# Optimization experiments

Measured on AMD Instinct MI355X. Metric: run time of the kernel, lower is better.

The kernel has to match this reference:

```python
import jax, jax.numpy as jnp
import numpy as np

B, T, D_IN, D_OUT, H = 2, 2048, 1024, 1024, 16
HD = D_OUT // H


def setup_inputs() -> dict:
    key = jax.random.key(0)
    ks = jax.random.split(key, 6)
    s_in = 1.0 / np.sqrt(D_IN)
    s_out = 1.0 / np.sqrt(D_OUT)
    return {
        "x": jax.random.normal(ks[0], (B, T, D_IN), dtype=jnp.float32),
        # torch nn.Linear stores weight as (out_features, in_features)
        "Wq": jax.random.uniform(ks[1], (D_OUT, D_IN), jnp.float32, -s_in, s_in),
        "Wk": jax.random.uniform(ks[2], (D_OUT, D_IN), jnp.float32, -s_in, s_in),
        "Wv": jax.random.uniform(ks[3], (D_OUT, D_IN), jnp.float32, -s_in, s_in),
        "Wo": jax.random.uniform(ks[4], (D_OUT, D_OUT), jnp.float32, -s_out, s_out),
        "bo": jax.random.uniform(ks[5], (D_OUT,), jnp.float32, -s_out, s_out),
    }


def reference(x, Wq, Wk, Wv, Wo, bo):
    b, t, _ = x.shape
    q = jnp.einsum("btd,ed->bte", x, Wq).reshape(b, t, H, HD).transpose(0, 2, 1, 3)
    k = jnp.einsum("btd,ed->bte", x, Wk).reshape(b, t, H, HD).transpose(0, 2, 1, 3)
    v = jnp.einsum("btd,ed->bte", x, Wv).reshape(b, t, H, HD).transpose(0, 2, 1, 3)
    # [b, h, q, k] materialized scores, masked then scaled (as in source)
    scores = jnp.einsum("bhqd,bhkd->bhqk", q, k)
    causal = jnp.triu(jnp.ones((t, t), dtype=bool), k=1)
    scores = jnp.where(causal, -jnp.inf, scores)
    attn = jax.nn.softmax(scores / jnp.sqrt(jnp.float32(HD)), axis=-1)
    ctx = jnp.einsum("bhqk,bhkd->bhqd", attn, v)
    # NOTE: the source does .view(b, t, d_out) WITHOUT transposing (b,h,t,hd)
    # back to (b,t,h,hd). We replicate that reshape faithfully.
    ctx = ctx.reshape(b, t, D_OUT)
    return jnp.einsum("btd,ed->bte", ctx, Wo) + bo
```

## Files before the change

kernel.cpp:

```cpp
#include <hip/hip_runtime.h>
#include <math.h>

#define BB 2
#define TT 2048
#define DD 1024
#define NH 16
#define HDD 64

typedef __attribute__((ext_vector_type(8))) short v8s;
typedef __attribute__((ext_vector_type(4))) short v4s;
typedef __attribute__((ext_vector_type(4))) float f32x4;

__device__ __forceinline__ unsigned short f2bf(float f) {
    union { float f; unsigned int u; } c; c.f = f;
    unsigned int r = c.u + 0x7FFF + ((c.u >> 16) & 1);
    return (unsigned short)(r >> 16);
}

__device__ __forceinline__ v4s pack_bf16x4(float a, float b, float c, float d) {
#if __has_builtin(__builtin_amdgcn_cvt_pk_bf16_f32)
    auto lo = __builtin_amdgcn_cvt_pk_bf16_f32(a, b);
    auto hi = __builtin_amdgcn_cvt_pk_bf16_f32(c, d);
    union { v4s v; struct { decltype(lo) l; decltype(hi) h; } p; } u;
    u.p.l = lo; u.p.h = hi;
    return u.v;
#else
    v4s r;
    r[0] = (short)f2bf(a); r[1] = (short)f2bf(b);
    r[2] = (short)f2bf(c); r[3] = (short)f2bf(d);
    return r;
#endif
}

__device__ __forceinline__ float fexp2(float x) {
#if __has_builtin(__builtin_amdgcn_exp2f)
    return __builtin_amdgcn_exp2f(x);
#else
    float r; asm("v_exp_f32 %0, %1" : "=v"(r) : "v"(x)); return r;
#endif
}

__device__ __forceinline__ void gload_lds16(const void* g, void* l) {
    __builtin_amdgcn_global_load_lds(
        (const __attribute__((address_space(1))) void*)g,
        (__attribute__((address_space(3))) void*)l, 16, 0, 0);
}

__device__ __forceinline__ f32x4 mfma16x16x16bf16(v4s a, v4s b, f32x4 c) {
#if __has_builtin(__builtin_amdgcn_mfma_f32_16x16x16bf16_1k)
    return __builtin_amdgcn_mfma_f32_16x16x16bf16_1k(a, b, c, 0, 0, 0);
#else
    f32x4 d;
    asm("v_mfma_f32_16x16x16_bf16 %0, %1, %2, %0"
        : "=v"(d) : "v"(a), "v"(b), "0"(c));
    return d;
#endif
}

__global__ __launch_bounds__(256) void cast5_kernel(
    const float* __restrict__ x, const float* __restrict__ wq,
    const float* __restrict__ wk, const float* __restrict__ wv,
    const float* __restrict__ wo,
    unsigned short* __restrict__ xo, unsigned short* __restrict__ wqo,
    unsigned short* __restrict__ wko, unsigned short* __restrict__ wvo,
    unsigned short* __restrict__ woo)
{
    const int tid = blockIdx.x * 256 + threadIdx.x;
    if (blockIdx.y == 0) {
        const int n4 = BB * TT * DD / 4;
#pragma unroll
        for (int p = 0; p < 4; ++p) {
            const int i = tid + (p << 18);
            if (i < n4) {
                float4 v = ((const float4*)x)[i];
                ushort4 o;
                o.x = f2bf(v.x); o.y = f2bf(v.y); o.z = f2bf(v.z); o.w = f2bf(v.w);
                ((ushort4*)xo)[i] = o;
            }
        }
    } else {
        const float* s; unsigned short* d;
        switch (blockIdx.y) {
            case 1: s = wq; d = wqo; break;
            case 2: s = wk; d = wko; break;
            case 3: s = wv; d = wvo; break;
            default: s = wo; d = woo; break;
        }
        float4 v = ((const float4*)s)[tid];
        ushort4 o;
        o.x = f2bf(v.x); o.y = f2bf(v.y); o.z = f2bf(v.z); o.w = f2bf(v.w);
        ((ushort4*)d)[tid] = o;
    }
}

__global__ __launch_bounds__(256, 3) void qkv_mfma(
    const unsigned short* __restrict__ x,
    const unsigned short* __restrict__ wq, const unsigned short* __restrict__ wk,
    const unsigned short* __restrict__ wv,
    unsigned short* __restrict__ qo, unsigned short* __restrict__ ko,
    unsigned short* __restrict__ vo)
{
    __shared__ unsigned short SMEM[24576];

    const int tid = threadIdx.x;
    const int lane = tid & 63;
    const int wid = tid >> 6;
    const int l15 = lane & 15, quad = lane >> 4;
    const int l7 = l15 & 7;

    const int m0 = blockIdx.x << 7;
    const int ny = blockIdx.y;
    const int which = ny >> 4;
    const int n0 = (ny & 15) << 6;
    const unsigned short* W = (which == 0) ? wq : (which == 1) ? wk : wv;

    const int wm = (wid >> 1) << 6;
    const int wn = (wid & 1) << 5;

    char* const smem = (char*)SMEM;

#define QKV_STAGE(k0, buf)                                                     \
    do {                                                                       \
        _Pragma("unroll") for (int p = 0; p < 4; ++p) {                        \
            const int f = (tid << 4) + (p << 12);                              \
            const int r = f >> 7;                                              \
            const int gc = ((((f >> 4) & 7) ^ (r & 7)) << 3);                  \
            gload_lds16(&x[(size_t)(m0 + r) * DD + (k0) + gc],                 \
                        smem + (buf) * 16384 + f);                             \
        }                                                                      \
        _Pragma("unroll") for (int p = 0; p < 2; ++p) {                        \
            const int f = (tid << 4) + (p << 12);                              \
            const int r = f >> 7;                                              \
            const int gc = ((((f >> 4) & 7) ^ (r & 7)) << 3);                  \
            gload_lds16(&W[(size_t)(n0 + r) * DD + (k0) + gc],                 \
                        smem + 32768 + (buf) * 8192 + f);                      \
        }                                                                      \
    } while (0)

    f32x4 acc[4][2] = {};

    QKV_STAGE(0, 0);
    __syncthreads();

    int cur = 0;
    for (int k0 = 0; k0 < DD; k0 += 64) {
        if (k0 + 64 < DD) QKV_STAGE(k0 + 64, cur ^ 1);

        const char* Ab = smem + cur * 16384;
        const char* Bb = smem + 32768 + cur * 8192;
#pragma unroll
        for (int h = 0; h < 2; ++h) {
            const int rc = (((h << 2) + quad) ^ l7) << 4;
            v8s af[4], bf[2];
#pragma unroll
            for (int i = 0; i < 4; ++i)
                af[i] = *(const v8s*)(Ab + (wm + (i << 4) + l15) * 128 + rc);
#pragma unroll
            for (int j = 0; j < 2; ++j)
                bf[j] = *(const v8s*)(Bb + (wn + (j << 4) + l15) * 128 + rc);
#pragma unroll
            for (int i = 0; i < 4; ++i)
#pragma unroll
                for (int j = 0; j < 2; ++j)
                    acc[i][j] = __builtin_amdgcn_mfma_f32_16x16x32_bf16(
                        af[i], bf[j], acc[i][j], 0, 0, 0);
        }

        __syncthreads();
        cur ^= 1;
    }
#undef QKV_STAGE

    if (which == 2) {
#pragma unroll
        for (int i = 0; i < 4; ++i)
#pragma unroll
            for (int j = 0; j < 2; ++j) {
                const int n = n0 + wn + (j << 4) + l15;
                const int h = n >> 6, hd = n & 63;
                const int mb = m0 + wm + (i << 4) + (quad << 2);
                const int b = mb >> 11, t = mb & 2047;
                ushort4 pk;
                pk.x = f2bf(acc[i][j][0]); pk.y = f2bf(acc[i][j][1]);
                pk.z = f2bf(acc[i][j][2]); pk.w = f2bf(acc[i][j][3]);
                *(ushort4*)&vo[((((size_t)(b * NH + h) << 6) + hd) << 11) + t] = pk;
            }
    } else {
        unsigned short* outp = (which == 0) ? qo : ko;
        const float sc = (which == 1) ? 0.18033688011112042f : 1.0f;
#pragma unroll
        for (int p = 0; p < 2; ++p) {
            __syncthreads();
            if ((wid >> 1) == p) {
#pragma unroll
                for (int i = 0; i < 4; ++i)
#pragma unroll
                    for (int j = 0; j < 2; ++j)
#pragma unroll
                        for (int r = 0; r < 4; ++r) {
                            const int row = (i << 4) + (quad << 2) + r;
                            SMEM[row * 72 + wn + (j << 4) + l15] = f2bf(acc[i][j][r] * sc);
                        }
            }
            __syncthreads();
            const int rr = tid >> 2;
            const int cg = (tid & 3) << 4;
            const int m = m0 + (p << 6) + rr;
            const int b = m >> 11, t = m & 2047;
#pragma unroll
            for (int k2 = 0; k2 < 2; ++k2) {
                const int col = cg + (k2 << 3);
                const int n = n0 + col;
                const int h = n >> 6, hd = n & 63;
                const uint4 val = *(const uint4*)&SMEM[rr * 72 + col];
                *(uint4*)&outp[(((size_t)(b * NH + h) * TT + t) << 6) + hd] = val;
            }
        }
    }
}

__global__ __launch_bounds__(256) void attn_mfma(
    const unsigned short* __restrict__ q, const unsigned short* __restrict__ k,
    const unsigned short* __restrict__ vt, unsigned short* __restrict__ ctx)
{
    __shared__ unsigned short Qs[64][64];
    __shared__ unsigned short Ks[2][64][64];
    __shared__ unsigned short Vts[2][64][64];

    const int tid = threadIdx.x;
    const int lane = tid & 63;
    const int wid = tid >> 6;
    const int l15 = lane & 15, quad = lane >> 4;
    const int r7 = (l15 & 7) << 3;

    const int bh = blockIdx.x;
    const int qt = 31 - (int)blockIdx.y;
    const int q0 = qt << 6;
    const int qrow = q0 + (wid << 4) + l15;

    const unsigned short* qb = q + (size_t)bh * TT * HDD;
    const unsigned short* kb = k + (size_t)bh * TT * HDD;
    const unsigned short* vb = vt + (size_t)bh * HDD * TT;
    unsigned short* cb = ctx + (size_t)bh * TT * HDD;

    const int cr = tid >> 3;
    const int cc = (tid & 7) << 3;
    const int cs = cc ^ ((cr & 7) << 3);

#pragma unroll
    for (int u = 0; u < 2; ++u) {
        const int r = cr + (u << 5);
        *(uint4*)&Qs[r][cs] = *(const uint4*)&qb[(size_t)(q0 + r) * HDD + cc];
    }
    {
        uint4 k0r = *(const uint4*)&kb[(size_t)cr * HDD + cc];
        uint4 k1r = *(const uint4*)&kb[(size_t)(cr + 32) * HDD + cc];
        uint4 v0r = *(const uint4*)&vb[((size_t)cr << 11) + cc];
        uint4 v1r = *(const uint4*)&vb[((size_t)(cr + 32) << 11) + cc];
        *(uint4*)&Ks[0][cr][cs] = k0r;
        *(uint4*)&Ks[0][cr + 32][cs] = k1r;
        *(uint4*)&Vts[0][cr][cs] = v0r;
        *(uint4*)&Vts[0][cr + 32][cs] = v1r;
    }
    __syncthreads();

    v8s qf[2];
#pragma unroll
    for (int c = 0; c < 2; ++c)
        qf[c] = *(const v8s*)&Qs[(wid << 4) + l15]
                               [(((c << 5) + (quad << 3)) ^ r7)];

    float m_i = -INFINITY, l_i = 0.f;
    f32x4 o[4] = {};

    for (int jt = 0; jt <= qt; ++jt) {
        const int cur = jt & 1;

        uint4 k0r, k1r, v0r, v1r;
        const bool pre = (jt < qt);
        if (pre) {
            const int kn = (jt + 1) << 6;
            k0r = *(const uint4*)&kb[(size_t)(kn + cr) * HDD + cc];
            k1r = *(const uint4*)&kb[(size_t)(kn + cr + 32) * HDD + cc];
            v0r = *(const uint4*)&vb[((size_t)cr << 11) + kn + cc];
            v1r = *(const uint4*)&vb[((size_t)(cr + 32) << 11) + kn + cc];
        }

        const int k0 = jt << 6;

        f32x4 s[4] = {};
        const int kc0 = (quad << 3) ^ r7;
#pragma unroll
        for (int m = 0; m < 4; ++m) {
            const v8s kf0 = *(const v8s*)&Ks[cur][(m << 4) + l15][kc0];
            const v8s kf1 = *(const v8s*)&Ks[cur][(m << 4) + l15][kc0 ^ 32];
            s[m] = __builtin_amdgcn_mfma_f32_16x16x32_bf16(kf0, qf[0], s[m], 0, 0, 0);
            s[m] = __builtin_amdgcn_mfma_f32_16x16x32_bf16(kf1, qf[1], s[m], 0, 0, 0);
        }

        if (jt == qt) {
#pragma unroll
            for (int m = 0; m < 4; ++m) {
                const int kc = k0 + (m << 4) + (quad << 2);
#pragma unroll
                for (int r = 0; r < 4; ++r)
                    if (kc + r > qrow) s[m][r] = -INFINITY;
            }
        }

        float mx = fmaxf(fmaxf(s[0][0], s[0][1]), fmaxf(s[0][2], s[0][3]));
        mx = fmaxf(mx, fmaxf(fmaxf(s[1][0], s[1][1]), fmaxf(s[1][2], s[1][3])));
        mx = fmaxf(mx, fmaxf(fmaxf(s[2][0], s[2][1]), fmaxf(s[2][2], s[2][3])));
        mx = fmaxf(mx, fmaxf(fmaxf(s[3][0], s[3][1]), fmaxf(s[3][2], s[3][3])));
        mx = fmaxf(mx, __shfl_xor(mx, 16));
        mx = fmaxf(mx, __shfl_xor(mx, 32));
        const float m_new = fmaxf(m_i, mx);
        const float alpha = fexp2(m_i - m_new);
        m_i = m_new;

        float sum = 0.f;
        v4s pf[4];
#pragma unroll
        for (int m = 0; m < 4; ++m) {
            const float p0 = fexp2(s[m][0] - m_new);
            const float p1 = fexp2(s[m][1] - m_new);
            const float p2 = fexp2(s[m][2] - m_new);
            const float p3 = fexp2(s[m][3] - m_new);
            sum += (p0 + p1) + (p2 + p3);
            pf[m] = pack_bf16x4(p0, p1, p2, p3);
        }
        sum += __shfl_xor(sum, 16);
        sum += __shfl_xor(sum, 32);
        l_i = l_i * alpha + sum;

#pragma unroll
        for (int m = 0; m < 4; ++m)
#pragma unroll
            for (int r = 0; r < 4; ++r)
                o[m][r] *= alpha;

#pragma unroll
        for (int m = 0; m < 4; ++m)
#pragma unroll
            for (int c = 0; c < 4; ++c) {
                const v4s vf = *(const v4s*)&Vts[cur][(m << 4) + l15]
                                                    [(((c << 4) + (quad << 2)) ^ r7)];
                o[m] = mfma16x16x16bf16(vf, pf[c], o[m]);
            }

        if (pre) {
            const int nxt = cur ^ 1;
            *(uint4*)&Ks[nxt][cr][cs] = k0r;
            *(uint4*)&Ks[nxt][cr + 32][cs] = k1r;
            *(uint4*)&Vts[nxt][cr][cs] = v0r;
            *(uint4*)&Vts[nxt][cr + 32][cs] = v1r;
        }
        __syncthreads();
    }

    const float linv = 1.f / l_i;
#pragma unroll
    for (int m = 0; m < 4; ++m) {
        ushort4 st;
        st.x = f2bf(o[m][0] * linv); st.y = f2bf(o[m][1] * linv);
        st.z = f2bf(o[m][2] * linv); st.w = f2bf(o[m][3] * linv);
        *(ushort4*)&cb[((size_t)qrow << 6) + (m << 4) + (quad << 2)] = st;
    }
}

__global__ __launch_bounds__(256, 3) void oproj_mfma(
    const unsigned short* __restrict__ c, const unsigned short* __restrict__ wo,
    const float* __restrict__ bo, float* __restrict__ out)
{
    __shared__ unsigned short SMEM[24576];

    const int tid = threadIdx.x;
    const int lane = tid & 63;
    const int wid = tid >> 6;
    const int l15 = lane & 15, quad = lane >> 4;
    const int l7 = l15 & 7;

    const int m0 = blockIdx.x << 7;
    const int n0 = blockIdx.y << 6;
    const int wm = (wid >> 1) << 6;
    const int wn = (wid & 1) << 5;

    char* const smem = (char*)SMEM;

#define OP_STAGE(k0, buf)                                                      \
    do {                                                                       \
        _Pragma("unroll") for (int p = 0; p < 4; ++p) {                        \
            const int f = (tid << 4) + (p << 12);                              \
            const int r = f >> 7;                                              \
            const int gc = ((((f >> 4) & 7) ^ (r & 7)) << 3);                  \
            gload_lds16(&c[(size_t)(m0 + r) * DD + (k0) + gc],                 \
                        smem + (buf) * 16384 + f);                             \
        }                                                                      \
        _Pragma("unroll") for (int p = 0; p < 2; ++p) {                        \
            const int f = (tid << 4) + (p << 12);                              \
            const int r = f >> 7;                                              \
            const int gc = ((((f >> 4) & 7) ^ (r & 7)) << 3);                  \
            gload_lds16(&wo[(size_t)(n0 + r) * DD + (k0) + gc],                \
                        smem + 32768 + (buf) * 8192 + f);                      \
        }                                                                      \
    } while (0)

    f32x4 acc[4][2] = {};

    OP_STAGE(0, 0);
    __syncthreads();

    int cur = 0;
    for (int k0 = 0; k0 < DD; k0 += 64) {
        if (k0 + 64 < DD) OP_STAGE(k0 + 64, cur ^ 1);

        const char* Ab = smem + cur * 16384;
        const char* Bb = smem + 32768 + cur * 8192;
#pragma unroll
        for (int h = 0; h < 2; ++h) {
            const int rc = (((h << 2) + quad) ^ l7) << 4;
            v8s af[4], bf[2];
#pragma unroll
            for (int i = 0; i < 4; ++i)
                af[i] = *(const v8s*)(Ab + (wm + (i << 4) + l15) * 128 + rc);
#pragma unroll
            for (int j = 0; j < 2; ++j)
                bf[j] = *(const v8s*)(Bb + (wn + (j << 4) + l15) * 128 + rc);
#pragma unroll
            for (int i = 0; i < 4; ++i)
#pragma unroll
                for (int j = 0; j < 2; ++j)
                    acc[i][j] = __builtin_amdgcn_mfma_f32_16x16x32_bf16(
                        af[i], bf[j], acc[i][j], 0, 0, 0);
        }

        __syncthreads();
        cur ^= 1;
    }
#undef OP_STAGE

#pragma unroll
    for (int j = 0; j < 2; ++j) {
        const int n = n0 + wn + (j << 4) + l15;
        const float bias = bo[n];
#pragma unroll
        for (int i = 0; i < 4; ++i) {
            const int mb = m0 + wm + (i << 4) + (quad << 2);
#pragma unroll
            for (int r = 0; r < 4; ++r)
                out[(size_t)(mb + r) * DD + n] = acc[i][j][r] + bias;
        }
    }
}

extern "C" void kernel_launch(void* const* d_in, const int* in_sizes, int n_in,
                              void* d_out, int out_size, void* d_ws, size_t ws_size,
                              hipStream_t stream) {
    const float* x  = (const float*)d_in[0];
    const float* Wq = (const float*)d_in[1];
    const float* Wk = (const float*)d_in[2];
    const float* Wv = (const float*)d_in[3];
    const float* Wo = (const float*)d_in[4];
    const float* bo = (const float*)d_in[5];
    float* out = (float*)d_out;

    const size_t NX = (size_t)BB * TT * DD;
    const size_t NW = (size_t)DD * DD;

    unsigned short* xb  = (unsigned short*)d_ws;
    unsigned short* wqb = xb + NX;
    unsigned short* wkb = wqb + NW;
    unsigned short* wvb = wkb + NW;
    unsigned short* wob = wvb + NW;
    unsigned short* qb  = wob + NW;
    unsigned short* kb  = qb + NX;
    unsigned short* vtb = kb + NX;
    unsigned short* cbuf = vtb + NX;

    cast5_kernel<<<dim3(1024, 5), 256, 0, stream>>>(x, Wq, Wk, Wv, Wo,
                                                    xb, wqb, wkb, wvb, wob);
    qkv_mfma<<<dim3(32, 48), 256, 0, stream>>>(xb, wqb, wkb, wvb, qb, kb, vtb);
    attn_mfma<<<dim3(32, 32), 256, 0, stream>>>(qb, kb, vtb, cbuf);
    oproj_mfma<<<dim3(32, 16), 256, 0, stream>>>(cbuf, wob, bo, out);
}
```

Before: 169.3 us.

## Widen attention key/value tile to 128 and load Q fragments from global

The attention kernel now processes 128 keys per iteration instead of 64. This halves the number of loop iterations, barriers and online-softmax rescale steps per query tile. The K/V shared buffers double in size and get new XOR swizzles, and the staging loads move into macros. Q fragments are read straight from global memory into registers rather than through a shared-memory tile. In exchange, LDS per block grows to 64KB and register pressure rises, which can lower occupancy, and the last block wastes work on fully masked keys when the query tile index is even.

Result: slower. 217.1 us (+28.3%).

```diff
diff --git a/kernel.cpp b/kernel.cpp
--- a/kernel.cpp
+++ b/kernel.cpp
@@ -223,19 +223,20 @@
     const unsigned short* __restrict__ q, const unsigned short* __restrict__ k,
     const unsigned short* __restrict__ vt, unsigned short* __restrict__ ctx)
 {
-    __shared__ unsigned short Qs[64][64];
-    __shared__ unsigned short Ks[2][64][64];
-    __shared__ unsigned short Vts[2][64][64];
+    __shared__ unsigned short Ks[2][128][64];
+    __shared__ unsigned short Vts[2][64][128];
 
     const int tid = threadIdx.x;
     const int lane = tid & 63;
     const int wid = tid >> 6;
     const int l15 = lane & 15, quad = lane >> 4;
     const int r7 = (l15 & 7) << 3;
+    const int rv = l15 << 3;
 
     const int bh = blockIdx.x;
     const int qt = 31 - (int)blockIdx.y;
     const int q0 = qt << 6;
+    const int nkb = (qt >> 1) + 1;
     const int qrow = q0 + (wid << 4) + l15;
 
     const unsigned short* qb = q + (size_t)bh * TT * HDD;
@@ -243,75 +244,76 @@
     const unsigned short* vb = vt + (size_t)bh * HDD * TT;
     unsigned short* cb = ctx + (size_t)bh * TT * HDD;
 
-    const int cr = tid >> 3;
-    const int cc = (tid & 7) << 3;
-    const int cs = cc ^ ((cr & 7) << 3);
-
-#pragma unroll
-    for (int u = 0; u < 2; ++u) {
-        const int r = cr + (u << 5);
-        *(uint4*)&Qs[r][cs] = *(const uint4*)&qb[(size_t)(q0 + r) * HDD + cc];
-    }
-    {
-        uint4 k0r = *(const uint4*)&kb[(size_t)cr * HDD + cc];
-        uint4 k1r = *(const uint4*)&kb[(size_t)(cr + 32) * HDD + cc];
-        uint4 v0r = *(const uint4*)&vb[((size_t)cr << 11) + cc];
-        uint4 v1r = *(const uint4*)&vb[((size_t)(cr + 32) << 11) + cc];
-        *(uint4*)&Ks[0][cr][cs] = k0r;
-        *(uint4*)&Ks[0][cr + 32][cs] = k1r;
-        *(uint4*)&Vts[0][cr][cs] = v0r;
-        *(uint4*)&Vts[0][cr + 32][cs] = v1r;
-    }
+    uint4 kr[4], vr[4];
+
+#define ATT_LOAD(kn)                                                           \
+    do {                                                                       \
+        _Pragma("unroll") for (int p = 0; p < 4; ++p) {                        \
+            const int f = (tid << 4) + (p << 12);                              \
+            const int krow = f >> 7, kch = (f >> 4) & 7;                       \
+            const int vrow = f >> 8, vch = (f >> 4) & 15;                      \
+            kr[p] = *(const uint4*)&kb[(size_t)((kn) + krow) * HDD + (kch << 3)]; \
+            vr[p] = *(const uint4*)&vb[((size_t)vrow << 11) + (kn) + (vch << 3)]; \
+        }                                                                      \
+    } while (0)
+
+#define ATT_PUBLISH(buf)                                                       \
+    do {                                                                       \
+        _Pragma("unroll") for (int p = 0; p < 4; ++p) {                        \
+            const int f = (tid << 4) + (p << 12);                              \
+            const int krow = f >> 7, kch = (f >> 4) & 7;                       \
+            const int vrow = f >> 8, vch = (f >> 4) & 15;                      \
+            *(uint4*)&Ks[buf][krow][(kch ^ (krow & 7)) << 3] = kr[p];          \
+            *(uint4*)&Vts[buf][vrow][(vch ^ (vrow & 15)) << 3] = vr[p];        \
+        }                                                                      \
+    } while (0)
+
+    ATT_LOAD(0);
+    ATT_PUBLISH(0);
+
+    v8s qf[2];
+#pragma unroll
+    for (int c = 0; c < 2; ++c)
+        qf[c] = *(const v8s*)&qb[(size_t)(q0 + (wid << 4) + l15) * HDD
+                                 + (c << 5) + (quad << 3)];
+
     __syncthreads();
-
-    v8s qf[2];
-#pragma unroll
-    for (int c = 0; c < 2; ++c)
-        qf[c] = *(const v8s*)&Qs[(wid << 4) + l15]
-                               [(((c << 5) + (quad << 3)) ^ r7)];
 
     float m_i = -INFINITY, l_i = 0.f;
     f32x4 o[4] = {};
 
-    for (int jt = 0; jt <= qt; ++jt) {
-        const int cur = jt & 1;
-
-        uint4 k0r, k1r, v0r, v1r;
-        const bool pre = (jt < qt);
-        if (pre) {
-            const int kn = (jt + 1) << 6;
-            k0r = *(const uint4*)&kb[(size_t)(kn + cr) * HDD + cc];
-            k1r = *(const uint4*)&kb[(size_t)(kn + cr + 32) * HDD + cc];
-            v0r = *(const uint4*)&vb[((size_t)cr << 11) + kn + cc];
-            v1r = *(const uint4*)&vb[((size_t)(cr + 32) << 11) + kn + cc];
-        }
-
-        const int k0 = jt << 6;
-
-        f32x4 s[4] = {};
+    for (int jb = 0; jb < nkb; ++jb) {
+        const int cur = jb & 1;
+        const bool pre = (jb + 1 < nkb);
+        if (pre) ATT_LOAD((jb + 1) << 7);
+
+        f32x4 s[8];
         const int kc0 = (quad << 3) ^ r7;
 #pragma unroll
-        for (int m = 0; m < 4; ++m) {
-            const v8s kf0 = *(const v8s*)&Ks[cur][(m << 4) + l15][kc0];
-            const v8s kf1 = *(const v8s*)&Ks[cur][(m << 4) + l15][kc0 ^ 32];
-            s[m] = __builtin_amdgcn_mfma_f32_16x16x32_bf16(kf0, qf[0], s[m], 0, 0, 0);
-            s[m] = __builtin_amdgcn_mfma_f32_16x16x32_bf16(kf1, qf[1], s[m], 0, 0, 0);
-        }
-
-        if (jt == qt) {
-#pragma unroll
-            for (int m = 0; m < 4; ++m) {
-                const int kc = k0 + (m << 4) + (quad << 2);
+        for (int mk = 0; mk < 8; ++mk) {
+            const v8s kf0 = *(const v8s*)&Ks[cur][(mk << 4) + l15][kc0];
+            const v8s kf1 = *(const v8s*)&Ks[cur][(mk << 4) + l15][kc0 ^ 32];
+            f32x4 t = {};
+            t = __builtin_amdgcn_mfma_f32_16x16x32_bf16(kf0, qf[0], t, 0, 0, 0);
+            t = __builtin_amdgcn_mfma_f32_16x16x32_bf16(kf1, qf[1], t, 0, 0, 0);
+            s[mk] = t;
+        }
+
+        if (jb == nkb - 1) {
+#pragma unroll
+            for (int mk = 0; mk < 8; ++mk) {
+                const int kc = (jb << 7) + (mk << 4) + (quad << 2);
 #pragma unroll
                 for (int r = 0; r < 4; ++r)
-                    if (kc + r > qrow) s[m][r] = -INFINITY;
-            }
-        }
-
-        float mx = fmaxf(fmaxf(s[0][0], s[0][1]), fmaxf(s[0][2], s[0][3]));
-        mx = fmaxf(mx, fmaxf(fmaxf(s[1][0], s[1][1]), fmaxf(s[1][2], s[1][3])));
-        mx = fmaxf(mx, fmaxf(fmaxf(s[2][0], s[2][1]), fmaxf(s[2][2], s[2][3])));
-        mx = fmaxf(mx, fmaxf(fmaxf(s[3][0], s[3][1]), fmaxf(s[3][2], s[3][3])));
+                    if (kc + r > qrow) s[mk][r] = -INFINITY;
+            }
+        }
+
+        float mx = -INFINITY;
+#pragma unroll
+        for (int mk = 0; mk < 8; ++mk)
+            mx = fmaxf(mx, fmaxf(fmaxf(s[mk][0], s[mk][1]),
+                                 fmaxf(s[mk][2], s[mk][3])));
         mx = fmaxf(mx, __shfl_xor(mx, 16));
         mx = fmaxf(mx, __shfl_xor(mx, 32));
         const float m_new = fmaxf(m_i, mx);
@@ -319,15 +321,15 @@
         m_i = m_new;
 
         float sum = 0.f;
-        v4s pf[4];
-#pragma unroll
-        for (int m = 0; m < 4; ++m) {
-            const float p0 = fexp2(s[m][0] - m_new);
-            const float p1 = fexp2(s[m][1] - m_new);
-            const float p2 = fexp2(s[m][2] - m_new);
-            const float p3 = fexp2(s[m][3] - m_new);
+        v4s pf[8];
+#pragma unroll
+        for (int mk = 0; mk < 8; ++mk) {
+            const float p0 = fexp2(s[mk][0] - m_new);
+            const float p1 = fexp2(s[mk][1] - m_new);
+            const float p2 = fexp2(s[mk][2] - m_new);
+            const float p3 = fexp2(s[mk][3] - m_new);
             sum += (p0 + p1) + (p2 + p3);
-            pf[m] = pack_bf16x4(p0, p1, p2, p3);
+            pf[mk] = pack_bf16x4(p0, p1, p2, p3);
         }
         sum += __shfl_xor(sum, 16);
         sum += __shfl_xor(sum, 32);
@@ -342,21 +344,17 @@
 #pragma unroll
         for (int m = 0; m < 4; ++m)
 #pragma unroll
-            for (int c = 0; c < 4; ++c) {
+            for (int c = 0; c < 8; ++c) {
                 const v4s vf = *(const v4s*)&Vts[cur][(m << 4) + l15]
-                                                    [(((c << 4) + (quad << 2)) ^ r7)];
+                                                    [(((c << 4) + (quad << 2)) ^ rv)];
                 o[m] = mfma16x16x16bf16(vf, pf[c], o[m]);
             }
 
-        if (pre) {
-            const int nxt = cur ^ 1;
-            *(uint4*)&Ks[nxt][cr][cs] = k0r;
-            *(uint4*)&Ks[nxt][cr + 32][cs] = k1r;
-            *(uint4*)&Vts[nxt][cr][cs] = v0r;
-            *(uint4*)&Vts[nxt][cr + 32][cs] = v1r;
-        }
+        if (pre) ATT_PUBLISH(cur ^ 1);
         __syncthreads();
     }
+#undef ATT_LOAD
+#undef ATT_PUBLISH
 
     const float linv = 1.f / l_i;
 #pragma unroll
```

## Unroll attention loop by two, use max3, MFMA row sums and setprio

Applied to the files above, without the earlier changes.

Unrolls the attention key-tile loop by two so the double-buffer index becomes a compile-time constant. It replaces the fmaxf reduction tree with v_max3_f32 inline asm and computes the softmax row sum with MFMAs against a ones vector instead of VALU adds plus shuffles. It also raises wave priority around the MFMA blocks with s_setprio. These moves shift work from VALU to the matrix unit and help interleave waves, at the cost of more code size and register pressure.

Result: no change. 171.3 us (+1.2%).

```diff
diff --git a/kernel.cpp b/kernel.cpp
--- a/kernel.cpp
+++ b/kernel.cpp
@@ -40,6 +40,12 @@
 #endif
 }
 
+__device__ __forceinline__ float fmax3(float a, float b, float c) {
+    float d;
+    asm("v_max3_f32 %0, %1, %2, %3" : "=v"(d) : "v"(a), "v"(b), "v"(c));
+    return d;
+}
+
 __device__ __forceinline__ void gload_lds16(const void* g, void* l) {
     __builtin_amdgcn_global_load_lds(
         (const __attribute__((address_space(1))) void*)g,
@@ -270,93 +276,94 @@
         qf[c] = *(const v8s*)&Qs[(wid << 4) + l15]
                                [(((c << 5) + (quad << 3)) ^ r7)];
 
+    const v4s vones = {0x3F80, 0x3F80, 0x3F80, 0x3F80};
     float m_i = -INFINITY, l_i = 0.f;
     f32x4 o[4] = {};
-
-    for (int jt = 0; jt <= qt; ++jt) {
-        const int cur = jt & 1;
-
-        uint4 k0r, k1r, v0r, v1r;
-        const bool pre = (jt < qt);
-        if (pre) {
-            const int kn = (jt + 1) << 6;
-            k0r = *(const uint4*)&kb[(size_t)(kn + cr) * HDD + cc];
-            k1r = *(const uint4*)&kb[(size_t)(kn + cr + 32) * HDD + cc];
-            v0r = *(const uint4*)&vb[((size_t)cr << 11) + kn + cc];
-            v1r = *(const uint4*)&vb[((size_t)(cr + 32) << 11) + kn + cc];
-        }
-
-        const int k0 = jt << 6;
-
-        f32x4 s[4] = {};
-        const int kc0 = (quad << 3) ^ r7;
-#pragma unroll
-        for (int m = 0; m < 4; ++m) {
-            const v8s kf0 = *(const v8s*)&Ks[cur][(m << 4) + l15][kc0];
-            const v8s kf1 = *(const v8s*)&Ks[cur][(m << 4) + l15][kc0 ^ 32];
-            s[m] = __builtin_amdgcn_mfma_f32_16x16x32_bf16(kf0, qf[0], s[m], 0, 0, 0);
-            s[m] = __builtin_amdgcn_mfma_f32_16x16x32_bf16(kf1, qf[1], s[m], 0, 0, 0);
-        }
-
-        if (jt == qt) {
-#pragma unroll
-            for (int m = 0; m < 4; ++m) {
-                const int kc = k0 + (m << 4) + (quad << 2);
-#pragma unroll
-                for (int r = 0; r < 4; ++r)
-                    if (kc + r > qrow) s[m][r] = -INFINITY;
-            }
-        }
-
-        float mx = fmaxf(fmaxf(s[0][0], s[0][1]), fmaxf(s[0][2], s[0][3]));
-        mx = fmaxf(mx, fmaxf(fmaxf(s[1][0], s[1][1]), fmaxf(s[1][2], s[1][3])));
-        mx = fmaxf(mx, fmaxf(fmaxf(s[2][0], s[2][1]), fmaxf(s[2][2], s[2][3])));
-        mx = fmaxf(mx, fmaxf(fmaxf(s[3][0], s[3][1]), fmaxf(s[3][2], s[3][3])));
-        mx = fmaxf(mx, __shfl_xor(mx, 16));
-        mx = fmaxf(mx, __shfl_xor(mx, 32));
-        const float m_new = fmaxf(m_i, mx);
-        const float alpha = fexp2(m_i - m_new);
-        m_i = m_new;
-
-        float sum = 0.f;
-        v4s pf[4];
-#pragma unroll
-        for (int m = 0; m < 4; ++m) {
-            const float p0 = fexp2(s[m][0] - m_new);
-            const float p1 = fexp2(s[m][1] - m_new);
-            const float p2 = fexp2(s[m][2] - m_new);
-            const float p3 = fexp2(s[m][3] - m_new);
-            sum += (p0 + p1) + (p2 + p3);
-            pf[m] = pack_bf16x4(p0, p1, p2, p3);
-        }
-        sum += __shfl_xor(sum, 16);
-        sum += __shfl_xor(sum, 32);
-        l_i = l_i * alpha + sum;
-
-#pragma unroll
-        for (int m = 0; m < 4; ++m)
-#pragma unroll
-            for (int r = 0; r < 4; ++r)
-                o[m][r] *= alpha;
-
-#pragma unroll
-        for (int m = 0; m < 4; ++m)
-#pragma unroll
-            for (int c = 0; c < 4; ++c) {
-                const v4s vf = *(const v4s*)&Vts[cur][(m << 4) + l15]
-                                                    [(((c << 4) + (quad << 2)) ^ r7)];
-                o[m] = mfma16x16x16bf16(vf, pf[c], o[m]);
-            }
-
-        if (pre) {
-            const int nxt = cur ^ 1;
-            *(uint4*)&Ks[nxt][cr][cs] = k0r;
-            *(uint4*)&Ks[nxt][cr + 32][cs] = k1r;
-            *(uint4*)&Vts[nxt][cr][cs] = v0r;
-            *(uint4*)&Vts[nxt][cr + 32][cs] = v1r;
-        }
-        __syncthreads();
-    }
+    const int kc0 = (quad << 3) ^ r7;
+
+#define ATT_BODY(JT, CUR)                                                      \
+    {                                                                          \
+        uint4 k0r, k1r, v0r, v1r;                                              \
+        const bool pre = ((JT) < qt);                                          \
+        if (pre) {                                                             \
+            const int kn = ((JT) + 1) << 6;                                    \
+            k0r = *(const uint4*)&kb[(size_t)(kn + cr) * HDD + cc];            \
+            k1r = *(const uint4*)&kb[(size_t)(kn + cr + 32) * HDD + cc];       \
+            v0r = *(const uint4*)&vb[((size_t)cr << 11) + kn + cc];            \
+            v1r = *(const uint4*)&vb[((size_t)(cr + 32) << 11) + kn + cc];     \
+        }                                                                      \
+        f32x4 s[4] = {};                                                       \
+        __builtin_amdgcn_s_setprio(1);                                         \
+        _Pragma("unroll") for (int m = 0; m < 4; ++m) {                        \
+            const v8s kf0 = *(const v8s*)&Ks[CUR][(m << 4) + l15][kc0];        \
+            const v8s kf1 = *(const v8s*)&Ks[CUR][(m << 4) + l15][kc0 ^ 32];   \
+            s[m] = __builtin_amdgcn_mfma_f32_16x16x32_bf16(kf0, qf[0], s[m], 0, 0, 0); \
+            s[m] = __builtin_amdgcn_mfma_f32_16x16x32_bf16(kf1, qf[1], s[m], 0, 0, 0); \
+        }                                                                      \
+        __builtin_amdgcn_s_setprio(0);                                         \
+        if ((JT) == qt) {                                                      \
+            _Pragma("unroll") for (int m = 0; m < 4; ++m) {                    \
+                const int kc = ((JT) << 6) + (m << 4) + (quad << 2);           \
+                _Pragma("unroll") for (int r = 0; r < 4; ++r)                  \
+                    if (kc + r > qrow) s[m][r] = -INFINITY;                    \
+            }                                                                  \
+        }                                                                      \
+        float mx = fmax3(s[0][0], s[0][1], s[0][2]);                           \
+        float mb2 = fmax3(s[0][3], s[1][0], s[1][1]);                          \
+        float mb3 = fmax3(s[1][2], s[1][3], s[2][0]);                          \
+        float mb4 = fmax3(s[2][1], s[2][2], s[2][3]);                          \
+        float mb5 = fmax3(s[3][0], s[3][1], s[3][2]);                          \
+        mx = fmax3(mx, mb2, mb3);                                              \
+        mb4 = fmax3(mb4, mb5, s[3][3]);                                        \
+        mx = fmaxf(mx, mb4);                                                   \
+        mx = fmaxf(mx, __shfl_xor(mx, 16));                                    \
+        mx = fmaxf(mx, __shfl_xor(mx, 32));                                    \
+        const float m_new = fmaxf(m_i, mx);                                    \
+        const float alpha = fexp2(m_i - m_new);                                \
+        m_i = m_new;                                                           \
+        v4s pf[4];                                                             \
+        _Pragma("unroll") for (int m = 0; m < 4; ++m) {                        \
+            const float p0 = fexp2(s[m][0] - m_new);                           \
+            const float p1 = fexp2(s[m][1] - m_new);                           \
+            const float p2 = fexp2(s[m][2] - m_new);                           \
+            const float p3 = fexp2(s[m][3] - m_new);                           \
+            pf[m] = pack_bf16x4(p0, p1, p2, p3);                               \
+        }                                                                      \
+        f32x4 ls = {};                                                         \
+        ls = mfma16x16x16bf16(vones, pf[0], ls);                               \
+        ls = mfma16x16x16bf16(vones, pf[1], ls);                               \
+        ls = mfma16x16x16bf16(vones, pf[2], ls);                               \
+        ls = mfma16x16x16bf16(vones, pf[3], ls);                               \
+        l_i = l_i * alpha + ls[0];                                             \
+        _Pragma("unroll") for (int m = 0; m < 4; ++m)                          \
+            _Pragma("unroll") for (int r = 0; r < 4; ++r)                      \
+                o[m][r] *= alpha;                                              \
+        __builtin_amdgcn_s_setprio(1);                                         \
+        _Pragma("unroll") for (int m = 0; m < 4; ++m)                          \
+            _Pragma("unroll") for (int c = 0; c < 4; ++c) {                    \
+                const v4s vf = *(const v4s*)&Vts[CUR][(m << 4) + l15]          \
+                                   [(((c << 4) + (quad << 2)) ^ r7)];          \
+                o[m] = mfma16x16x16bf16(vf, pf[c], o[m]);                      \
+            }                                                                  \
+        __builtin_amdgcn_s_setprio(0);                                         \
+        if (pre) {                                                             \
+            *(uint4*)&Ks[1 - (CUR)][cr][cs] = k0r;                             \
+            *(uint4*)&Ks[1 - (CUR)][cr + 32][cs] = k1r;                        \
+            *(uint4*)&Vts[1 - (CUR)][cr][cs] = v0r;                            \
+            *(uint4*)&Vts[1 - (CUR)][cr + 32][cs] = v1r;                       \
+        }                                                                      \
+        __syncthreads();                                                       \
+    }
+
+    int jt = 0;
+    for (; jt + 1 <= qt; jt += 2) {
+        ATT_BODY(jt, 0);
+        ATT_BODY(jt + 1, 1);
+    }
+    if (jt <= qt) {
+        ATT_BODY(jt, 0);
+    }
+#undef ATT_BODY
 
     const float linv = 1.f / l_i;
 #pragma unroll
```
